# Kernel tuning notes

Measured on AMD Instinct MI355X. Metric: run time of the kernel, lower is better.

## Reference

```python
import jax, jax.numpy as jnp
import numpy as np

B, L, D, H = 2, 2048, 1024, 16
DH = D // H


def setup_inputs() -> dict:
    key = jax.random.key(0)
    ks = jax.random.split(key, 12)
    s = 0.02
    return {
        "q": jax.random.normal(ks[0], (B, L, D), jnp.float32),
        "k": jax.random.normal(ks[1], (B, L, D), jnp.float32),
        "v": jax.random.normal(ks[2], (B, L, D), jnp.float32),
        "pos_enc": jax.random.normal(ks[3], (L + 1, D), jnp.float32),
        "Wq": jax.random.normal(ks[4], (D, D), jnp.float32) * s,
        "bq": jnp.zeros((D,), jnp.float32),
        "Wk": jax.random.normal(ks[5], (D, D), jnp.float32) * s,
        "bk": jnp.zeros((D,), jnp.float32),
        "Wv": jax.random.normal(ks[6], (D, D), jnp.float32) * s,
        "bv": jnp.zeros((D,), jnp.float32),
        "Wo": jax.random.normal(ks[7], (D, D), jnp.float32) * s,
        "bo": jnp.zeros((D,), jnp.float32),
        "r_w_bias": jax.random.normal(ks[8], (H, 1, DH), jnp.float32) * s,
        "r_r_bias": jax.random.normal(ks[9], (H, 1, DH), jnp.float32) * s,
        "r_kernel": jax.random.normal(ks[10], (H, D, DH), jnp.float32) * s,
    }


def reference(q, k, v, pos_enc, Wq, bq, Wk, bk, Wv, bv, Wo, bo,
              r_w_bias, r_r_bias, r_kernel):
    b, lq, d = q.shape
    h, _, dh = r_w_bias.shape
    lk = k.shape[1]
    scale = dh ** -0.5

    # q/k/v projections, then split heads: [b, l, d] -> [b, h, l, dh]
    qh = (q @ Wq + bq).reshape(b, lq, h, dh).transpose(0, 2, 1, 3)
    kh = (k @ Wk + bk).reshape(b, lk, h, dh).transpose(0, 2, 1, 3)
    vh = (v @ Wv + bv).reshape(b, lk, h, dh).transpose(0, 2, 1, 3)

    # content scores with global content bias (Transformer-XL r_w_bias)
    scores = jnp.einsum('bhqd,bhkd->bhqk', qh + r_w_bias, kh) * scale

    # relative-position term: pos_enc [p, d] @ r_kernel [h, d, dh] -> [h, p, dh]
    pe = jnp.einsum('pd,hde->hpe', pos_enc, r_kernel)
    rel = jnp.einsum('bhqd,hpd->bhqp', qh + r_r_bias, pe) * scale  # [b,h,lq,p]
    p = rel.shape[-1]
    shift = 1 + (lq != lk)
    # rel-shift trick: reshape with swapped last two dims, drop first `shift`
    # rows, reshape back, keep first lk columns
    rel = rel.reshape(b, h, p, lq)[:, :, shift:, :]
    rel = rel.reshape(b, h, lq, p - shift)[..., :lk]
    scores = scores + rel

    # causal mask (key_cache is None path): subtract 1e7 on strict upper triangle
    causal_mask = jnp.triu(jnp.ones((lq, lk), dtype=bool), 1)
    scores = scores - causal_mask * 1e7

    out = jnp.einsum('bhqk,bhkd->bhqd', jax.nn.softmax(scores, axis=-1), vh)
    out = out.transpose(0, 2, 1, 3).reshape(b, lq, d)  # merge heads
    return out @ Wo + bo
```

## Files before the change

### kernel.cpp

```cpp
#include <hip/hip_runtime.h>
#include <hip/hip_bf16.h>

typedef __attribute__((ext_vector_type(8))) short bf16x8;
typedef __attribute__((ext_vector_type(4))) float f32x4;
typedef __attribute__((ext_vector_type(16))) float f32x16;
typedef unsigned short u16;
typedef unsigned int u32;

#define DEV static __device__ __forceinline__

DEV u16 f2us(float x) {
  __hip_bfloat16 h = __float2bfloat16(x);
  union { __hip_bfloat16 h; u16 u; } c; c.h = h; return c.u;
}
DEV float us2f(u16 u) {
  union { __hip_bfloat16 h; u16 u; } c; c.u = u;
  return __bfloat162float(c.h);
}
DEV f32x16 mfma32(bf16x8 a, bf16x8 b, f32x16 c) {
  return __builtin_amdgcn_mfma_f32_32x32x16_bf16(a, b, c, 0, 0, 0);
}
DEV u32 pkbf(float a, float b) {
  return (u32)f2us(a) | ((u32)f2us(b) << 16);
}
DEV void gl16(const u16* g, u16* l) {
  __builtin_amdgcn_global_load_lds(
      (const __attribute__((address_space(1))) unsigned int*)(g),
      (__attribute__((address_space(3))) unsigned int*)(l), 16, 0, 0);
}

constexpr int PE_ROWS = 2144;
constexpr int PE_M    = 2176;
constexpr float QSCALE = 0.125f;

constexpr size_t SZ_QKV  = (size_t)4096 * 1024 * 2;
constexpr size_t SZ_W    = (size_t)1024 * 1024 * 2;
constexpr size_t SZ_POSB = (size_t)PE_M * 1024 * 2;
constexpr size_t OFF_QB   = 0;
constexpr size_t OFF_KB   = OFF_QB  + SZ_QKV;
constexpr size_t OFF_VB   = OFF_KB  + SZ_QKV;
constexpr size_t OFF_WQT  = OFF_VB  + SZ_QKV;
constexpr size_t OFF_WKT  = OFF_WQT + SZ_W;
constexpr size_t OFF_WVT  = OFF_WKT + SZ_W;
constexpr size_t OFF_WOT  = OFF_WVT + SZ_W;
constexpr size_t OFF_RKT  = OFF_WOT + SZ_W;
constexpr size_t OFF_POSB = OFF_RKT + SZ_W;
constexpr size_t OFF_QW   = OFF_POSB + SZ_POSB;
constexpr size_t OFF_QR   = OFF_QW  + SZ_QKV;
constexpr size_t OFF_KH   = OFF_QR  + SZ_QKV;
constexpr size_t OFF_VT   = OFF_KH  + SZ_QKV;
constexpr size_t OFF_PEH  = OFF_VT  + SZ_QKV;
constexpr size_t OFF_ATTNB = OFF_QB;

__global__ __launch_bounds__(256)
void k_f2b_all(const float4* __restrict__ q, const float4* __restrict__ k,
               const float4* __restrict__ v, const float4* __restrict__ pos,
               u16* __restrict__ qb, u16* __restrict__ kb,
               u16* __restrict__ vb, u16* __restrict__ posb)
{
  const int bid = blockIdx.x;
  const float4* src; u16* dst; int i; int n4in, n4tot;
  if (bid < 4096)       { src = q;   dst = qb;   i = bid * 256 + threadIdx.x;           n4in = 1048576; n4tot = 1048576; }
  else if (bid < 8192)  { src = k;   dst = kb;   i = (bid - 4096) * 256 + threadIdx.x;  n4in = 1048576; n4tot = 1048576; }
  else if (bid < 12288) { src = v;   dst = vb;   i = (bid - 8192) * 256 + threadIdx.x;  n4in = 1048576; n4tot = 1048576; }
  else                  { src = pos; dst = posb; i = (bid - 12288) * 256 + threadIdx.x; n4in = 524544;  n4tot = 557056; }
  if (i >= n4tot) return;
  float4 val;
  if (i < n4in) val = src[i];
  else { val.x = val.y = val.z = val.w = 0.f; }
  ushort4 o;
  o.x = f2us(val.x); o.y = f2us(val.y); o.z = f2us(val.z); o.w = f2us(val.w);
  *reinterpret_cast<ushort4*>(dst + (size_t)i * 4) = o;
}

struct TcPtrs { const float *i0, *i1, *i2, *i3; u16 *o0, *o1, *o2, *o3; };

__global__ __launch_bounds__(256)
void k_tconv4(TcPtrs tp)
{
  const int z = blockIdx.z;
  const float* in = (z == 0) ? tp.i0 : (z == 1) ? tp.i1 : (z == 2) ? tp.i2 : tp.i3;
  u16* out = (z == 0) ? tp.o0 : (z == 1) ? tp.o1 : (z == 2) ? tp.o2 : tp.o3;
  __shared__ float t[32][33];
  const int kb0 = blockIdx.x * 32, nb0 = blockIdx.y * 32;
  const int tx = threadIdx.x & 31, ty = threadIdx.x >> 5;
#pragma unroll
  for (int r = 0; r < 32; r += 8)
    t[ty + r][tx] = in[(size_t)(kb0 + ty + r) * 1024 + nb0 + tx];
  __syncthreads();
#pragma unroll
  for (int r = 0; r < 32; r += 8)
    out[(size_t)(nb0 + ty + r) * 1024 + kb0 + tx] = f2us(t[tx][ty + r]);
}

__global__ __launch_bounds__(256)
void k_rkt(const float* __restrict__ rk, u16* __restrict__ out) {
  __shared__ float t[32][33];
  const int h = blockIdx.z;
  const int eb0 = blockIdx.x * 32, db0 = blockIdx.y * 32;
  const int tx = threadIdx.x & 31, ty = threadIdx.x >> 5;
#pragma unroll
  for (int r = 0; r < 32; r += 8)
    t[ty + r][tx] = rk[(size_t)h * 65536 + (size_t)(db0 + ty + r) * 64 + eb0 + tx];
  __syncthreads();
#pragma unroll
  for (int r = 0; r < 32; r += 8)
    out[(size_t)(h * 64 + eb0 + ty + r) * 1024 + db0 + tx] = f2us(t[tx][ty + r]);
}

struct ProjPtrs {
  const u16 *A0, *A1, *A2, *A3;
  const u16 *B0, *B1, *B2, *B3;
  const float *bias0, *bias1, *bias2;
  const float *rwb, *rrb;
  u16 *Qw, *Qr, *Kh, *Vt, *PEh;
};

__global__ __launch_bounds__(256)
void k_gemm_proj(ProjPtrs pp)
{
  const int z = blockIdx.z;
  if (z == 3 && blockIdx.y >= PE_M / 128) return;
  const u16* A  = (z == 0) ? pp.A0 : (z == 1) ? pp.A1 : (z == 2) ? pp.A2 : pp.A3;
  const u16* Bt = (z == 0) ? pp.B0 : (z == 1) ? pp.B1 : (z == 2) ? pp.B2 : pp.B3;

  __shared__ __attribute__((aligned(16))) u16 As[128 * 32];
  __shared__ __attribute__((aligned(16))) u16 Bs[128 * 32];
  const int tid  = threadIdx.x;
  const int lane = tid & 63;
  const int wave = tid >> 6;
  const int bm = blockIdx.y * 128;
  const int bn = blockIdx.x * 128;
  const int wr = (wave >> 1) * 64;
  const int wc = (wave & 1) * 64;
  const int fr = lane & 15;
  const int fk = (lane >> 4) * 8;

  f32x4 zero = {0.f, 0.f, 0.f, 0.f};
  f32x4 acc[4][4];
#pragma unroll
  for (int m = 0; m < 4; ++m)
#pragma unroll
    for (int n = 0; n < 4; ++n) acc[m][n] = zero;

  const int cA = wave * 2;
  const u16* gA = A  + (size_t)(bm + cA * 16 + (lane >> 2)) * 1024 + (lane & 3) * 8;
  const u16* gB = Bt + (size_t)(bn + cA * 16 + (lane >> 2)) * 1024 + (lane & 3) * 8;
  u16* lA = As + cA * 512;
  u16* lB = Bs + cA * 512;

  for (int k0 = 0; k0 < 1024; k0 += 32) {
    gl16(gA + k0, lA);
    gl16(gA + 16 * 1024 + k0, lA + 512);
    gl16(gB + k0, lB);
    gl16(gB + 16 * 1024 + k0, lB + 512);
    __syncthreads();
    bf16x8 af[4], bfv[4];
#pragma unroll
    for (int m = 0; m < 4; ++m) af[m]  = *(const bf16x8*)(&As[(wr + m * 16 + fr) * 32 + fk]);
#pragma unroll
    for (int n = 0; n < 4; ++n) bfv[n] = *(const bf16x8*)(&Bs[(wc + n * 16 + fr) * 32 + fk]);
#pragma unroll
    for (int m = 0; m < 4; ++m)
#pragma unroll
      for (int n = 0; n < 4; ++n)
        acc[m][n] = __builtin_amdgcn_mfma_f32_16x16x32_bf16(af[m], bfv[n], acc[m][n], 0, 0, 0);
    __syncthreads();
  }

#pragma unroll
  for (int m = 0; m < 4; ++m)
#pragma unroll
    for (int n = 0; n < 4; ++n)
#pragma unroll
      for (int r = 0; r < 4; ++r) {
        const int grow = bm + wr + m * 16 + (lane >> 4) * 4 + r;
        const int gcol = bn + wc + n * 16 + fr;
        float v = acc[m][n][r];
        const int b_ = grow >> 11, l_ = grow & 2047;
        const int h_ = gcol >> 6,  e_ = gcol & 63;
        if (z == 0) {
          v += pp.bias0[gcol];
          const size_t o = (((size_t)(b_ * 16 + h_) * 2048 + l_) << 6) + e_;
          pp.Qw[o] = f2us((v + pp.rwb[gcol]) * QSCALE);
          pp.Qr[o] = f2us((v + pp.rrb[gcol]) * QSCALE);
        } else if (z == 1) {
          v += pp.bias1[gcol];
          const size_t o = (((size_t)(b_ * 16 + h_) * 2048 + l_) << 6) + e_;
          pp.Kh[o] = f2us(v);
        } else if (z == 2) {
          v += pp.bias2[gcol];
          const size_t o = (((size_t)(b_ * 16 + h_) * 64 + e_) << 11) + l_;
          pp.Vt[o] = f2us(v);
        } else {
          if (grow < PE_ROWS) {
            const size_t o = ((size_t)h_ * PE_ROWS + grow) * 64 + e_;
            pp.PEh[o] = f2us(v);
          }
        }
      }
}

__global__ __launch_bounds__(256)
void k_gemm_o(const u16* __restrict__ A, const u16* __restrict__ Bt,
              const float* __restrict__ bias, float* __restrict__ outf)
{
  __shared__ __attribute__((aligned(16))) u16 As[128 * 32];
  __shared__ __attribute__((aligned(16))) u16 Bs[128 * 32];
  const int tid  = threadIdx.x;
  const int lane = tid & 63;
  const int wave = tid >> 6;
  const int bm = blockIdx.y * 128;
  const int bn = blockIdx.x * 128;
  const int wr = (wave >> 1) * 64;
  const int wc = (wave & 1) * 64;
  const int fr = lane & 15;
  const int fk = (lane >> 4) * 8;

  f32x4 zero = {0.f, 0.f, 0.f, 0.f};
  f32x4 acc[4][4];
#pragma unroll
  for (int m = 0; m < 4; ++m)
#pragma unroll
    for (int n = 0; n < 4; ++n) acc[m][n] = zero;

  const int cA = wave * 2;
  const u16* gA = A  + (size_t)(bm + cA * 16 + (lane >> 2)) * 1024 + (lane & 3) * 8;
  const u16* gB = Bt + (size_t)(bn + cA * 16 + (lane >> 2)) * 1024 + (lane & 3) * 8;
  u16* lA = As + cA * 512;
  u16* lB = Bs + cA * 512;

  for (int k0 = 0; k0 < 1024; k0 += 32) {
    gl16(gA + k0, lA);
    gl16(gA + 16 * 1024 + k0, lA + 512);
    gl16(gB + k0, lB);
    gl16(gB + 16 * 1024 + k0, lB + 512);
    __syncthreads();
    bf16x8 af[4], bfv[4];
#pragma unroll
    for (int m = 0; m < 4; ++m) af[m]  = *(const bf16x8*)(&As[(wr + m * 16 + fr) * 32 + fk]);
#pragma unroll
    for (int n = 0; n < 4; ++n) bfv[n] = *(const bf16x8*)(&Bs[(wc + n * 16 + fr) * 32 + fk]);
#pragma unroll
    for (int m = 0; m < 4; ++m)
#pragma unroll
      for (int n = 0; n < 4; ++n)
        acc[m][n] = __builtin_amdgcn_mfma_f32_16x16x32_bf16(af[m], bfv[n], acc[m][n], 0, 0, 0);
    __syncthreads();
  }

#pragma unroll
  for (int m = 0; m < 4; ++m)
#pragma unroll
    for (int n = 0; n < 4; ++n)
#pragma unroll
      for (int r = 0; r < 4; ++r) {
        const int grow = bm + wr + m * 16 + (lane >> 4) * 4 + r;
        const int gcol = bn + wc + n * 16 + fr;
        outf[(size_t)grow * 1024 + gcol] = acc[m][n][r] + bias[gcol];
      }
}


#define PV_HALF(WARR)                                                          \
  {                                                                            \
    _Pragma("unroll")                                                          \
    for (int kvs = 0; kvs < 2; ++kvs) {                                        \
      u32 snd0 = hi ? WARR[4 * kvs]     : WARR[4 * kvs + 2];                   \
      u32 snd1 = hi ? WARR[4 * kvs + 1] : WARR[4 * kvs + 3];                   \
      u32 r0 = (u32)__shfl_xor((int)snd0, 32);                                 \
      u32 r1 = (u32)__shfl_xor((int)snd1, 32);                                 \
      union { u32 u[4]; bf16x8 v; } pf;                                        \
      pf.u[0] = hi ? r0 : WARR[4 * kvs];                                       \
      pf.u[1] = hi ? r1 : WARR[4 * kvs + 1];                                   \
      pf.u[2] = hi ? WARR[4 * kvs + 2] : r0;                                   \
      pf.u[3] = hi ? WARR[4 * kvs + 3] : r1;                                   \
      bf16x8 v0_ = *(const bf16x8*)(V_h + (size_t)l31 * 2048 + c0h_            \
                                    + kvs * 16 + hi * 8);                      \
      bf16x8 v1_ = *(const bf16x8*)(V_h + (size_t)(32 + l31) * 2048 + c0h_     \
                                    + kvs * 16 + hi * 8);                      \
      Oc0 = mfma32(v0_, pf.v, Oc0);                                            \
      Oc1 = mfma32(v1_, pf.v, Oc1);                                            \
    }                                                                          \
  }

#define ATTN_HALF(q0v, c0_, KT)                                                \
  {                                                                            \
    const int c0h_ = (c0_) + (KT) * 32;                                        \
    f32x16 sv_ = {};                                                           \
    {                                                                          \
      bf16x8 kf_[4];                                                           \
      _Pragma("unroll")                                                        \
      for (int kk = 0; kk < 4; ++kk)                                           \
        kf_[kk] = *(const bf16x8*)(K_h + (size_t)(c0h_ + l31) * 64 + kk * 16   \
                                   + hi * 8);                                  \
      _Pragma("unroll")                                                        \
      for (int kk = 0; kk < 4; ++kk) sv_ = mfma32(kf_[kk], qwf[kk], sv_);      \
    }                                                                          \
    _Pragma("unroll")                                                          \
    for (int r = 0; r < 16; ++r) {                                             \
      const int pat = (r & 3) + 8 * (r >> 2) + 4 * hi;                         \
      float x = sv_[r] + us2f(Ew[l31][(KT) * 32 + pat + 31 - l31]);            \
      if (c0h_ + pat > (q0v) + l31) x = -1e30f;                                \
      sv_[r] = x;                                                              \
    }                                                                          \
    float mx_ = sv_[0];                                                        \
    _Pragma("unroll")                                                          \
    for (int r = 1; r < 16; ++r) mx_ = fmaxf(mx_, sv_[r]);                     \
    mx_ = fmaxf(mx_, __shfl_xor(mx_, 32));                                     \
    const float mn_ = fmaxf(mrun, mx_);                                        \
    const float al_ = __expf(mrun - mn_);                                      \
    mrun = mn_;                                                                \
    float rsum_ = 0.f;                                                         \
    u32 wa_[8];                                                                \
    _Pragma("unroll")                                                          \
    for (int g8 = 0; g8 < 8; ++g8) {                                           \
      float pa_ = __expf(sv_[2 * g8] - mn_);                                   \
      float pb_ = __expf(sv_[2 * g8 + 1] - mn_);                               \
      u16 ua_ = f2us(pa_), ub_ = f2us(pb_);                                    \
      rsum_ += us2f(ua_) + us2f(ub_);                                          \
      wa_[g8] = (u32)ua_ | ((u32)ub_ << 16);                                   \
    }                                                                          \
    ls = ls * al_ + rsum_ + __shfl_xor(rsum_, 32);                             \
    Oc0 *= al_;                                                                \
    Oc1 *= al_;                                                                \
    PV_HALF(wa_)                                                               \
  }

#define ATTN_STEP(q0v, stv)                                                    \
  {                                                                            \
    const int c0_ = (stv) * 64;                                                \
    const int Jb_ = 2048 + c0_ - (q0v) - 31;                                   \
    _Pragma("unroll")                                                          \
    for (int tau = 0; tau < 3; ++tau) {                                        \
      f32x16 e_ = {};                                                          \
      {                                                                        \
        bf16x8 pe_[4];                                                         \
        _Pragma("unroll")                                                      \
        for (int kk = 0; kk < 4; ++kk)                                         \
          pe_[kk] = *(const bf16x8*)(PE_h + (size_t)(Jb_ + tau * 32 + l31)     \
                                     * 64 + kk * 16 + hi * 8);                 \
        _Pragma("unroll")                                                      \
        for (int kk = 0; kk < 4; ++kk) e_ = mfma32(pe_[kk], qrf[kk], e_);      \
      }                                                                        \
      _Pragma("unroll")                                                        \
      for (int g4 = 0; g4 < 4; ++g4) {                                         \
        uint2 w2_;                                                             \
        w2_.x = pkbf(e_[4 * g4 + 0], e_[4 * g4 + 1]);                          \
        w2_.y = pkbf(e_[4 * g4 + 2], e_[4 * g4 + 3]);                          \
        *(uint2*)(&Ew[l31][tau * 32 + 8 * g4 + 4 * hi]) = w2_;                 \
      }                                                                        \
    }                                                                          \
    ATTN_HALF(q0v, c0_, 0)                                                     \
    ATTN_HALF(q0v, c0_, 1)                                                     \
  }

#define OBROUND(PRE, SCL)                                                      \
  {                                                                            \
    _Pragma("unroll")                                                          \
    for (int g4 = 0; g4 < 4; ++g4) {                                           \
      float* pb0 = &Obuf[l31][8 * g4 + 4 * hi];                                \
      float* pb1 = &Obuf[l31][32 + 8 * g4 + 4 * hi];                           \
      float2 a0 = *(float2*)pb0,       a1 = *(float2*)(pb0 + 2);               \
      float2 b0 = *(float2*)pb1,       b1 = *(float2*)(pb1 + 2);               \
      a0.x = a0.x * (PRE) + Oc0[4 * g4 + 0] * (SCL);                           \
      a0.y = a0.y * (PRE) + Oc0[4 * g4 + 1] * (SCL);                           \
      a1.x = a1.x * (PRE) + Oc0[4 * g4 + 2] * (SCL);                           \
      a1.y = a1.y * (PRE) + Oc0[4 * g4 + 3] * (SCL);                           \
      b0.x = b0.x * (PRE) + Oc1[4 * g4 + 0] * (SCL);                           \
      b0.y = b0.y * (PRE) + Oc1[4 * g4 + 1] * (SCL);                           \
      b1.x = b1.x * (PRE) + Oc1[4 * g4 + 2] * (SCL);                           \
      b1.y = b1.y * (PRE) + Oc1[4 * g4 + 3] * (SCL);                           \
      *(float2*)pb0 = a0; *(float2*)(pb0 + 2) = a1;                            \
      *(float2*)pb1 = b0; *(float2*)(pb1 + 2) = b1;                            \
    }                                                                          \
  }

__global__ __launch_bounds__(256, 4)
void k_attn(const u16* __restrict__ Qw, const u16* __restrict__ Qr,
            const u16* __restrict__ Kh, const u16* __restrict__ Vt,
            const u16* __restrict__ PEh, u16* __restrict__ attnb)
{
  const int bid = blockIdx.x;
  const int xcd = bid & 7, s = bid >> 3;
  const int p = s & 31, g = s >> 5;
  const int hb = xcd + 8 * g;
  const int h = hb & 15, b = hb >> 4;
  const int wave = threadIdx.x >> 6, lane = threadIdx.x & 63;
  const int l31 = lane & 31, hi = lane >> 5;

  const int qtL = 63 - p, qtS = p;
  const int q0L = qtL * 32, q0S = qtS * 32;
  const int nstL = qtL / 2 + 1;

  const u16* Qw_h = Qw + (size_t)hb * (2048 * 64);
  const u16* Qr_h = Qr + (size_t)hb * (2048 * 64);
  const u16* K_h  = Kh + (size_t)hb * (2048 * 64);
  const u16* V_h  = Vt + (size_t)hb * (64 * 2048);
  const u16* PE_h = PEh + (size_t)h * (PE_ROWS * 64);

  __shared__ __attribute__((aligned(16))) u16 Elds_all[4][32][100];
  __shared__ float Obuf[32][66];
  __shared__ float mlb[2][4][2][32];
  u16 (*Ew)[100] = Elds_all[wave];

  const int lo  = wave ? 9 + 8 * (wave - 1) : 0;
  const int hiE = lo + (wave ? 8 : 9);
  const int la0 = lo;
  const int la1 = hiE < nstL ? hiE : nstL;
  const int lb0 = lo > nstL ? lo : nstL;
  const int lb1 = hiE;
  const bool hasL = la1 > la0;
  const bool hasS = lb1 > lb0;
  const bool crossing = hasL && hasS;

  const f32x16 vzero = {};
  f32x16 Oc0 = {}, Oc1 = {};
  float mrun = -1e30f, ls = 0.f;
  bf16x8 qwf[4], qrf[4];

  if (hasL) {
#pragma unroll
    for (int kk = 0; kk < 4; ++kk) {
      qwf[kk] = *(const bf16x8*)(Qw_h + (size_t)(q0L + l31) * 64 + kk * 16 + hi * 8);
      qrf[kk] = *(const bf16x8*)(Qr_h + (size_t)(q0L + l31) * 64 + kk * 16 + hi * 8);
    }
    for (int st = la0; st < la1; ++st) ATTN_STEP(q0L, st)
  }
  if (crossing) {
    OBROUND(0.f, 1.f)
    if (hi == 0) { mlb[0][wave][0][l31] = mrun; mlb[0][wave][1][l31] = ls; }
    Oc0 = vzero; Oc1 = vzero; mrun = -1e30f; ls = 0.f;
  }
  if (hasS) {
#pragma unroll
    for (int kk = 0; kk < 4; ++kk) {
      qwf[kk] = *(const bf16x8*)(Qw_h + (size_t)(q0S + l31) * 64 + kk * 16 + hi * 8);
      qrf[kk] = *(const bf16x8*)(Qr_h + (size_t)(q0S + l31) * 64 + kk * 16 + hi * 8);
    }
    for (int st = lb0 - nstL; st < lb1 - nstL; ++st) ATTN_STEP(q0S, st)
  }

  if (hi == 0) {
    if (crossing) {
      mlb[1][wave][0][l31] = mrun; mlb[1][wave][1][l31] = ls;
    } else if (hasL) {
      mlb[0][wave][0][l31] = mrun;  mlb[0][wave][1][l31] = ls;
      mlb[1][wave][0][l31] = -1e30f; mlb[1][wave][1][l31] = 0.f;
    } else {
      mlb[1][wave][0][l31] = mrun;  mlb[1][wave][1][l31] = ls;
      mlb[0][wave][0][l31] = -1e30f; mlb[0][wave][1][l31] = 0.f;
    }
  }
  __syncthreads();

  const bool cwExists = (nstL != 17) && (nstL != 25);
  const int  cw = (nstL < 25) ? 2 : 3;

  const float mstL = fmaxf(fmaxf(mlb[0][0][0][l31], mlb[0][1][0][l31]),
                           fmaxf(mlb[0][2][0][l31], mlb[0][3][0][l31]));
  if (wave == 0) {
    const float preL = cwExists ? __expf(mlb[0][cw][0][l31] - mstL) : 0.f;
    const float scl = __expf(mrun - mstL);
    OBROUND(preL, scl)
  }
  __syncthreads();
  if (wave == 1) {
    const float scl = __expf(mrun - mstL);
    OBROUND(1.f, scl)
  }
  __syncthreads();
  if (wave == 2 && hasL && !crossing) {
    const float scl = __expf(mrun - mstL);
    OBROUND(1.f, scl)
  }
  __syncthreads();
  if (wave == 0) {
    float lst = 0.f;
#pragma unroll
    for (int w = 0; w < 4; ++w)
      lst += mlb[0][w][1][l31] * __expf(mlb[0][w][0][l31] - mstL);
    const float inv = 1.f / lst;
    const size_t orow = ((size_t)(b * 2048 + q0L + l31)) * 1024 + h * 64 + hi * 32;
#pragma unroll
    for (int j4 = 0; j4 < 32; j4 += 4) {
      float2 t0 = *(float2*)&Obuf[l31][hi * 32 + j4];
      float2 t1 = *(float2*)&Obuf[l31][hi * 32 + j4 + 2];
      ushort4 st;
      st.x = f2us(t0.x * inv); st.y = f2us(t0.y * inv);
      st.z = f2us(t1.x * inv); st.w = f2us(t1.y * inv);
      *(ushort4*)(attnb + orow + j4) = st;
    }
  }
  __syncthreads();

  const float mstS = fmaxf(mlb[1][2][0][l31], mlb[1][3][0][l31]);
  if (wave == 2 && hasS) {
    const float scl = __expf(mrun - mstS);
    OBROUND(0.f, scl)
  }
  __syncthreads();
  if (wave == 3) {
    const float scl = __expf(mrun - mstS);
    const float pre = (nstL < 25) ? 1.f : 0.f;
    OBROUND(pre, scl)
  }
  __syncthreads();
  if (wave == 1) {
    float lst = mlb[1][2][1][l31] * __expf(mlb[1][2][0][l31] - mstS)
              + mlb[1][3][1][l31] * __expf(mlb[1][3][0][l31] - mstS);
    const float inv = 1.f / lst;
    const size_t orow = ((size_t)(b * 2048 + q0S + l31)) * 1024 + h * 64 + hi * 32;
#pragma unroll
    for (int j4 = 0; j4 < 32; j4 += 4) {
      float2 t0 = *(float2*)&Obuf[l31][hi * 32 + j4];
      float2 t1 = *(float2*)&Obuf[l31][hi * 32 + j4 + 2];
      ushort4 st;
      st.x = f2us(t0.x * inv); st.y = f2us(t0.y * inv);
      st.z = f2us(t1.x * inv); st.w = f2us(t1.y * inv);
      *(ushort4*)(attnb + orow + j4) = st;
    }
  }
}

extern "C" void kernel_launch(void* const* d_in, const int* in_sizes, int n_in,
                              void* d_out, int out_size, void* d_ws, size_t ws_size,
                              hipStream_t stream)
{
  const float* q   = (const float*)d_in[0];
  const float* k   = (const float*)d_in[1];
  const float* v   = (const float*)d_in[2];
  const float* pos = (const float*)d_in[3];
  const float* Wq  = (const float*)d_in[4];
  const float* bq  = (const float*)d_in[5];
  const float* Wk  = (const float*)d_in[6];
  const float* bk  = (const float*)d_in[7];
  const float* Wv  = (const float*)d_in[8];
  const float* bv  = (const float*)d_in[9];
  const float* Wo  = (const float*)d_in[10];
  const float* bo  = (const float*)d_in[11];
  const float* rwb = (const float*)d_in[12];
  const float* rrb = (const float*)d_in[13];
  const float* rk  = (const float*)d_in[14];

  char* ws = (char*)d_ws;
  u16* qb    = (u16*)(ws + OFF_QB);
  u16* kb    = (u16*)(ws + OFF_KB);
  u16* vb    = (u16*)(ws + OFF_VB);
  u16* Wqt   = (u16*)(ws + OFF_WQT);
  u16* Wkt   = (u16*)(ws + OFF_WKT);
  u16* Wvt   = (u16*)(ws + OFF_WVT);
  u16* Wot   = (u16*)(ws + OFF_WOT);
  u16* Rkt   = (u16*)(ws + OFF_RKT);
  u16* posb  = (u16*)(ws + OFF_POSB);
  u16* Qw    = (u16*)(ws + OFF_QW);
  u16* Qr    = (u16*)(ws + OFF_QR);
  u16* Kh    = (u16*)(ws + OFF_KH);
  u16* Vt    = (u16*)(ws + OFF_VT);
  u16* PEh   = (u16*)(ws + OFF_PEH);
  u16* attnb = (u16*)(ws + OFF_ATTNB);
  float* outf = (float*)d_out;

  k_f2b_all<<<dim3(14464), 256, 0, stream>>>((const float4*)q, (const float4*)k,
                                             (const float4*)v, (const float4*)pos,
                                             qb, kb, vb, posb);
  TcPtrs tp;
  tp.i0 = Wq; tp.i1 = Wk; tp.i2 = Wv; tp.i3 = Wo;
  tp.o0 = Wqt; tp.o1 = Wkt; tp.o2 = Wvt; tp.o3 = Wot;
  k_tconv4<<<dim3(32, 32, 4), 256, 0, stream>>>(tp);
  k_rkt<<<dim3(2, 32, 16), 256, 0, stream>>>(rk, Rkt);

  ProjPtrs pp;
  pp.A0 = qb;  pp.A1 = kb;  pp.A2 = vb;  pp.A3 = posb;
  pp.B0 = Wqt; pp.B1 = Wkt; pp.B2 = Wvt; pp.B3 = Rkt;
  pp.bias0 = bq; pp.bias1 = bk; pp.bias2 = bv;
  pp.rwb = rwb; pp.rrb = rrb;
  pp.Qw = Qw; pp.Qr = Qr; pp.Kh = Kh; pp.Vt = Vt; pp.PEh = PEh;
  k_gemm_proj<<<dim3(8, 32, 4), 256, 0, stream>>>(pp);

  k_attn<<<dim3(1024), 256, 0, stream>>>(Qw, Qr, Kh, Vt, PEh, attnb);

  k_gemm_o<<<dim3(8, 32), 256, 0, stream>>>(attnb, Wot, bo, outf);
}
```

Baseline: 247.4 us.

## Merge prep kernels, reuse rel-pos tile across steps, use exp2 and mask skip

Folds the three preprocessing launches (bf16 conversion, weight transposes, r_kernel transpose) into a single kernel to save launch overhead. In attention, the third positional-encoding tile of each step is kept in registers and reused as the first tile of the next step, so each step computes two PE MFMA tiles instead of three. Causal masking is skipped for tiles entirely below the diagonal, V fragments are loaded early next to the K loads, and the softmax uses v_exp_f32 (exp2) with log2(e) folded into the Q scale. The stray label in the Rkt loop looks odd but is harmless; the cross-step register carry adds register pressure.

```diff
diff --git a/kernel.cpp b/kernel.cpp
--- a/kernel.cpp
+++ b/kernel.cpp
@@ -23,6 +23,11 @@
 DEV u32 pkbf(float a, float b) {
   return (u32)f2us(a) | ((u32)f2us(b) << 16);
 }
+DEV float fexp2(float x) {
+  float r;
+  asm("v_exp_f32 %0, %1" : "=v"(r) : "v"(x));
+  return r;
+}
 DEV void gl16(const u16* g, u16* l) {
   __builtin_amdgcn_global_load_lds(
       (const __attribute__((address_space(1))) unsigned int*)(g),
@@ -31,7 +36,7 @@
 
 constexpr int PE_ROWS = 2144;
 constexpr int PE_M    = 2176;
-constexpr float QSCALE = 0.125f;
+constexpr float QSC2 = 0.125f * 1.4426950408889634f;
 
 constexpr size_t SZ_QKV  = (size_t)4096 * 1024 * 2;
 constexpr size_t SZ_W    = (size_t)1024 * 1024 * 2;
@@ -52,60 +57,62 @@
 constexpr size_t OFF_PEH  = OFF_VT  + SZ_QKV;
 constexpr size_t OFF_ATTNB = OFF_QB;
 
+struct PrepPtrs {
+  const float4 *q, *k, *v, *pos;
+  u16 *qb, *kb, *vb, *posb;
+  const float *Wq, *Wk, *Wv, *Wo, *rk;
+  u16 *Wqt, *Wkt, *Wvt, *Wot, *Rkt;
+};
+
 __global__ __launch_bounds__(256)
-void k_f2b_all(const float4* __restrict__ q, const float4* __restrict__ k,
-               const float4* __restrict__ v, const float4* __restrict__ pos,
-               u16* __restrict__ qb, u16* __restrict__ kb,
-               u16* __restrict__ vb, u16* __restrict__ posb)
+void k_prep(PrepPtrs P)
 {
+  __shared__ float t[32][33];
   const int bid = blockIdx.x;
-  const float4* src; u16* dst; int i; int n4in, n4tot;
-  if (bid < 4096)       { src = q;   dst = qb;   i = bid * 256 + threadIdx.x;           n4in = 1048576; n4tot = 1048576; }
-  else if (bid < 8192)  { src = k;   dst = kb;   i = (bid - 4096) * 256 + threadIdx.x;  n4in = 1048576; n4tot = 1048576; }
-  else if (bid < 12288) { src = v;   dst = vb;   i = (bid - 8192) * 256 + threadIdx.x;  n4in = 1048576; n4tot = 1048576; }
-  else                  { src = pos; dst = posb; i = (bid - 12288) * 256 + threadIdx.x; n4in = 524544;  n4tot = 557056; }
-  if (i >= n4tot) return;
-  float4 val;
-  if (i < n4in) val = src[i];
-  else { val.x = val.y = val.z = val.w = 0.f; }
-  ushort4 o;
-  o.x = f2us(val.x); o.y = f2us(val.y); o.z = f2us(val.z); o.w = f2us(val.w);
-  *reinterpret_cast<ushort4*>(dst + (size_t)i * 4) = o;
-}
-
-struct TcPtrs { const float *i0, *i1, *i2, *i3; u16 *o0, *o1, *o2, *o3; };
-
-__global__ __launch_bounds__(256)
-void k_tconv4(TcPtrs tp)
-{
-  const int z = blockIdx.z;
-  const float* in = (z == 0) ? tp.i0 : (z == 1) ? tp.i1 : (z == 2) ? tp.i2 : tp.i3;
-  u16* out = (z == 0) ? tp.o0 : (z == 1) ? tp.o1 : (z == 2) ? tp.o2 : tp.o3;
-  __shared__ float t[32][33];
-  const int kb0 = blockIdx.x * 32, nb0 = blockIdx.y * 32;
+  if (bid < 14464) {
+    const float4* src; u16* dst; int i, n4in, n4tot;
+    if (bid < 4096)       { src = P.q;   dst = P.qb;   i = bid * 256 + threadIdx.x;           n4in = 1048576; n4tot = 1048576; }
+    else if (bid < 8192)  { src = P.k;   dst = P.kb;   i = (bid - 4096) * 256 + threadIdx.x;  n4in = 1048576; n4tot = 1048576; }
+    else if (bid < 12288) { src = P.v;   dst = P.vb;   i = (bid - 8192) * 256 + threadIdx.x;  n4in = 1048576; n4tot = 1048576; }
+    else                  { src = P.pos; dst = P.posb; i = (bid - 12288) * 256 + threadIdx.x; n4in = 524544;  n4tot = 557056; }
+    if (i >= n4tot) return;
+    float4 val;
+    if (i < n4in) val = src[i];
+    else { val.x = val.y = val.z = val.w = 0.f; }
+    ushort4 o;
+    o.x = f2us(val.x); o.y = f2us(val.y); o.z = f2us(val.z); o.w = f2us(val.w);
+    *reinterpret_cast<ushort4*>(dst + (size_t)i * 4) = o;
+    return;
+  }
   const int tx = threadIdx.x & 31, ty = threadIdx.x >> 5;
-#pragma unroll
-  for (int r = 0; r < 32; r += 8)
-    t[ty + r][tx] = in[(size_t)(kb0 + ty + r) * 1024 + nb0 + tx];
-  __syncthreads();
-#pragma unroll
-  for (int r = 0; r < 32; r += 8)
-    out[(size_t)(nb0 + ty + r) * 1024 + kb0 + tx] = f2us(t[tx][ty + r]);
-}
-
-__global__ __launch_bounds__(256)
-void k_rkt(const float* __restrict__ rk, u16* __restrict__ out) {
-  __shared__ float t[32][33];
-  const int h = blockIdx.z;
-  const int eb0 = blockIdx.x * 32, db0 = blockIdx.y * 32;
-  const int tx = threadIdx.x & 31, ty = threadIdx.x >> 5;
-#pragma unroll
-  for (int r = 0; r < 32; r += 8)
-    t[ty + r][tx] = rk[(size_t)h * 65536 + (size_t)(db0 + ty + r) * 64 + eb0 + tx];
-  __syncthreads();
-#pragma unroll
-  for (int r = 0; r < 32; r += 8)
-    out[(size_t)(h * 64 + eb0 + ty + r) * 1024 + db0 + tx] = f2us(t[tx][ty + r]);
+  if (bid < 18560) {
+    const int tt = bid - 14464;
+    const int z = tt >> 10, rr = tt & 1023;
+    const float* in = (z == 0) ? P.Wq : (z == 1) ? P.Wk : (z == 2) ? P.Wv : P.Wo;
+    u16* out = (z == 0) ? P.Wqt : (z == 1) ? P.Wkt : (z == 2) ? P.Wvt : P.Wot;
+    const int kb0 = (rr & 31) * 32, nb0 = (rr >> 5) * 32;
+#pragma unroll
+    for (int r = 0; r < 32; r += 8)
+      t[ty + r][tx] = in[(size_t)(kb0 + ty + r) * 1024 + nb0 + tx];
+    __syncthreads();
+#pragma unroll
+    for (int r = 0; r < 32; r += 8)
+      out[(size_t)(nb0 + ty + r) * 1024 + kb0 + tx] = f2us(t[tx][ty + r]);
+    return;
+  }
+  {
+    const int tt = bid - 18560;
+    const int e = tt & 1, d = (tt >> 1) & 31, h = tt >> 6;
+    const int eb0 = e * 32, db0 = d * 32;
+#pragma unroll
+    for (int r = 0; r < 32; r += 8)
+      t[ty + r][tx] = P.rk[(size_t)h * 65536 + (size_t)(db0 + ty + r) * 64 + eb0 + tx];
+    __syncthreads();
+#pragma unroll
+    for (int r = 0; r < 32; r += 8)
+      out_rkt_store:
+      P.Rkt[(size_t)(h * 64 + eb0 + ty + r) * 1024 + db0 + tx] = f2us(t[tx][ty + r]);
+  }
 }
 
 struct ProjPtrs {
@@ -182,8 +189,8 @@
         if (z == 0) {
           v += pp.bias0[gcol];
           const size_t o = (((size_t)(b_ * 16 + h_) * 2048 + l_) << 6) + e_;
-          pp.Qw[o] = f2us((v + pp.rwb[gcol]) * QSCALE);
-          pp.Qr[o] = f2us((v + pp.rrb[gcol]) * QSCALE);
+          pp.Qw[o] = f2us((v + pp.rwb[gcol]) * QSC2);
+          pp.Qr[o] = f2us((v + pp.rrb[gcol]) * QSC2);
         } else if (z == 1) {
           v += pp.bias1[gcol];
           const size_t o = (((size_t)(b_ * 16 + h_) * 2048 + l_) << 6) + e_;
@@ -262,61 +269,55 @@
 }
 
 
-#define PV_HALF(WARR)                                                          \
-  {                                                                            \
-    _Pragma("unroll")                                                          \
-    for (int kvs = 0; kvs < 2; ++kvs) {                                        \
-      u32 snd0 = hi ? WARR[4 * kvs]     : WARR[4 * kvs + 2];                   \
-      u32 snd1 = hi ? WARR[4 * kvs + 1] : WARR[4 * kvs + 3];                   \
-      u32 r0 = (u32)__shfl_xor((int)snd0, 32);                                 \
-      u32 r1 = (u32)__shfl_xor((int)snd1, 32);                                 \
-      union { u32 u[4]; bf16x8 v; } pf;                                        \
-      pf.u[0] = hi ? r0 : WARR[4 * kvs];                                       \
-      pf.u[1] = hi ? r1 : WARR[4 * kvs + 1];                                   \
-      pf.u[2] = hi ? WARR[4 * kvs + 2] : r0;                                   \
-      pf.u[3] = hi ? WARR[4 * kvs + 3] : r1;                                   \
-      bf16x8 v0_ = *(const bf16x8*)(V_h + (size_t)l31 * 2048 + c0h_            \
-                                    + kvs * 16 + hi * 8);                      \
-      bf16x8 v1_ = *(const bf16x8*)(V_h + (size_t)(32 + l31) * 2048 + c0h_     \
-                                    + kvs * 16 + hi * 8);                      \
-      Oc0 = mfma32(v0_, pf.v, Oc0);                                            \
-      Oc1 = mfma32(v1_, pf.v, Oc1);                                            \
-    }                                                                          \
-  }
-
 #define ATTN_HALF(q0v, c0_, KT)                                                \
   {                                                                            \
     const int c0h_ = (c0_) + (KT) * 32;                                        \
     f32x16 sv_ = {};                                                           \
+    bf16x8 vpa_[4];                                                            \
     {                                                                          \
       bf16x8 kf_[4];                                                           \
       _Pragma("unroll")                                                        \
       for (int kk = 0; kk < 4; ++kk)                                           \
         kf_[kk] = *(const bf16x8*)(K_h + (size_t)(c0h_ + l31) * 64 + kk * 16   \
                                    + hi * 8);                                  \
+      vpa_[0] = *(const bf16x8*)(V_h + (size_t)l31 * 2048 + c0h_ + hi * 8);    \
+      vpa_[1] = *(const bf16x8*)(V_h + (size_t)(32 + l31) * 2048 + c0h_        \
+                                 + hi * 8);                                    \
+      vpa_[2] = *(const bf16x8*)(V_h + (size_t)l31 * 2048 + c0h_ + 16          \
+                                 + hi * 8);                                    \
+      vpa_[3] = *(const bf16x8*)(V_h + (size_t)(32 + l31) * 2048 + c0h_ + 16   \
+                                 + hi * 8);                                    \
       _Pragma("unroll")                                                        \
       for (int kk = 0; kk < 4; ++kk) sv_ = mfma32(kf_[kk], qwf[kk], sv_);      \
     }                                                                          \
-    _Pragma("unroll")                                                          \
-    for (int r = 0; r < 16; ++r) {                                             \
-      const int pat = (r & 3) + 8 * (r >> 2) + 4 * hi;                         \
-      float x = sv_[r] + us2f(Ew[l31][(KT) * 32 + pat + 31 - l31]);            \
-      if (c0h_ + pat > (q0v) + l31) x = -1e30f;                                \
-      sv_[r] = x;                                                              \
+    if (c0h_ + 31 > (q0v)) {                                                   \
+      _Pragma("unroll")                                                        \
+      for (int r = 0; r < 16; ++r) {                                           \
+        const int pat = (r & 3) + 8 * (r >> 2) + 4 * hi;                       \
+        float x = sv_[r] + us2f(Ew[l31][(KT) * 32 + pat + 31 - l31]);          \
+        if (c0h_ + pat > (q0v) + l31) x = -1e30f;                              \
+        sv_[r] = x;                                                            \
+      }                                                                        \
+    } else {                                                                   \
+      _Pragma("unroll")                                                        \
+      for (int r = 0; r < 16; ++r) {                                           \
+        const int pat = (r & 3) + 8 * (r >> 2) + 4 * hi;                       \
+        sv_[r] += us2f(Ew[l31][(KT) * 32 + pat + 31 - l31]);                   \
+      }                                                                        \
     }                                                                          \
     float mx_ = sv_[0];                                                        \
     _Pragma("unroll")                                                          \
     for (int r = 1; r < 16; ++r) mx_ = fmaxf(mx_, sv_[r]);                     \
     mx_ = fmaxf(mx_, __shfl_xor(mx_, 32));                                     \
     const float mn_ = fmaxf(mrun, mx_);                                        \
-    const float al_ = __expf(mrun - mn_);                                      \
+    const float al_ = fexp2(mrun - mn_);                                       \
     mrun = mn_;                                                                \
     float rsum_ = 0.f;                                                         \
     u32 wa_[8];                                                                \
     _Pragma("unroll")                                                          \
     for (int g8 = 0; g8 < 8; ++g8) {                                           \
-      float pa_ = __expf(sv_[2 * g8] - mn_);                                   \
-      float pb_ = __expf(sv_[2 * g8 + 1] - mn_);                               \
+      float pa_ = fexp2(sv_[2 * g8] - mn_);                                    \
+      float pb_ = fexp2(sv_[2 * g8 + 1] - mn_);                                \
       u16 ua_ = f2us(pa_), ub_ = f2us(pb_);                                    \
       rsum_ += us2f(ua_) + us2f(ub_);                                          \
       wa_[g8] = (u32)ua_ | ((u32)ub_ << 16);                                   \
@@ -324,7 +325,40 @@
     ls = ls * al_ + rsum_ + __shfl_xor(rsum_, 32);                             \
     Oc0 *= al_;                                                                \
     Oc1 *= al_;                                                                \
-    PV_HALF(wa_)                                                               \
+    _Pragma("unroll")                                                          \
+    for (int kvs = 0; kvs < 2; ++kvs) {                                        \
+      u32 snd0 = hi ? wa_[4 * kvs]     : wa_[4 * kvs + 2];                     \
+      u32 snd1 = hi ? wa_[4 * kvs + 1] : wa_[4 * kvs + 3];                     \
+      u32 r0 = (u32)__shfl_xor((int)snd0, 32);                                 \
+      u32 r1 = (u32)__shfl_xor((int)snd1, 32);                                 \
+      union { u32 u[4]; bf16x8 v; } pf;                                        \
+      pf.u[0] = hi ? r0 : wa_[4 * kvs];                                        \
+      pf.u[1] = hi ? r1 : wa_[4 * kvs + 1];                                    \
+      pf.u[2] = hi ? wa_[4 * kvs + 2] : r0;                                    \
+      pf.u[3] = hi ? wa_[4 * kvs + 3] : r1;                                    \
+      Oc0 = mfma32(vpa_[2 * kvs], pf.v, Oc0);                                  \
+      Oc1 = mfma32(vpa_[2 * kvs + 1], pf.v, Oc1);                              \
+    }                                                                          \
+  }
+
+#define SEG_PROLOGUE(q0v, s0v)                                                 \
+  {                                                                            \
+    const int Jb_ = 2048 + (s0v) * 64 - (q0v) - 31;                            \
+    f32x16 e_ = {};                                                            \
+    {                                                                          \
+      bf16x8 pe_[4];                                                           \
+      _Pragma("unroll")                                                        \
+      for (int kk = 0; kk < 4; ++kk)                                           \
+        pe_[kk] = *(const bf16x8*)(PE_h + (size_t)(Jb_ + l31) * 64 + kk * 16   \
+                                   + hi * 8);                                  \
+      _Pragma("unroll")                                                        \
+      for (int kk = 0; kk < 4; ++kk) e_ = mfma32(pe_[kk], qrf[kk], e_);        \
+    }                                                                          \
+    _Pragma("unroll")                                                          \
+    for (int g4 = 0; g4 < 4; ++g4) {                                           \
+      cr[2 * g4]     = pkbf(e_[4 * g4 + 0], e_[4 * g4 + 1]);                   \
+      cr[2 * g4 + 1] = pkbf(e_[4 * g4 + 2], e_[4 * g4 + 3]);                   \
+    }                                                                          \
   }
 
 #define ATTN_STEP(q0v, stv)                                                    \
@@ -332,14 +366,18 @@
     const int c0_ = (stv) * 64;                                                \
     const int Jb_ = 2048 + c0_ - (q0v) - 31;                                   \
     _Pragma("unroll")                                                          \
-    for (int tau = 0; tau < 3; ++tau) {                                        \
+    for (int g4 = 0; g4 < 4; ++g4) {                                           \
+      uint2 w2_; w2_.x = cr[2 * g4]; w2_.y = cr[2 * g4 + 1];                   \
+      *(uint2*)(&Ew[l31][8 * g4 + 4 * hi]) = w2_;                              \
+    }                                                                          \
+    {                                                                          \
       f32x16 e_ = {};                                                          \
       {                                                                        \
         bf16x8 pe_[4];                                                         \
         _Pragma("unroll")                                                      \
         for (int kk = 0; kk < 4; ++kk)                                         \
-          pe_[kk] = *(const bf16x8*)(PE_h + (size_t)(Jb_ + tau * 32 + l31)     \
-                                     * 64 + kk * 16 + hi * 8);                 \
+          pe_[kk] = *(const bf16x8*)(PE_h + (size_t)(Jb_ + 32 + l31) * 64      \
+                                     + kk * 16 + hi * 8);                      \
         _Pragma("unroll")                                                      \
         for (int kk = 0; kk < 4; ++kk) e_ = mfma32(pe_[kk], qrf[kk], e_);      \
       }                                                                        \
@@ -348,7 +386,26 @@
         uint2 w2_;                                                             \
         w2_.x = pkbf(e_[4 * g4 + 0], e_[4 * g4 + 1]);                          \
         w2_.y = pkbf(e_[4 * g4 + 2], e_[4 * g4 + 3]);                          \
-        *(uint2*)(&Ew[l31][tau * 32 + 8 * g4 + 4 * hi]) = w2_;                 \
+        *(uint2*)(&Ew[l31][32 + 8 * g4 + 4 * hi]) = w2_;                       \
+      }                                                                        \
+    }                                                                          \
+    {                                                                          \
+      f32x16 e_ = {};                                                          \
+      {                                                                        \
+        bf16x8 pe_[4];                                                         \
+        _Pragma("unroll")                                                      \
+        for (int kk = 0; kk < 4; ++kk)                                         \
+          pe_[kk] = *(const bf16x8*)(PE_h + (size_t)(Jb_ + 64 + l31) * 64      \
+                                     + kk * 16 + hi * 8);                      \
+        _Pragma("unroll")                                                      \
+        for (int kk = 0; kk < 4; ++kk) e_ = mfma32(pe_[kk], qrf[kk], e_);      \
+      }                                                                        \
+      _Pragma("unroll")                                                        \
+      for (int g4 = 0; g4 < 4; ++g4) {                                         \
+        cr[2 * g4]     = pkbf(e_[4 * g4 + 0], e_[4 * g4 + 1]);                 \
+        cr[2 * g4 + 1] = pkbf(e_[4 * g4 + 2], e_[4 * g4 + 3]);                 \
+        uint2 w2_; w2_.x = cr[2 * g4]; w2_.y = cr[2 * g4 + 1];                 \
+        *(uint2*)(&Ew[l31][64 + 8 * g4 + 4 * hi]) = w2_;                       \
       }                                                                        \
     }                                                                          \
     ATTN_HALF(q0v, c0_, 0)                                                     \
@@ -418,6 +475,7 @@
   f32x16 Oc0 = {}, Oc1 = {};
   float mrun = -1e30f, ls = 0.f;
   bf16x8 qwf[4], qrf[4];
+  u32 cr[8];
 
   if (hasL) {
 #pragma unroll
@@ -425,6 +483,7 @@
       qwf[kk] = *(const bf16x8*)(Qw_h + (size_t)(q0L + l31) * 64 + kk * 16 + hi * 8);
       qrf[kk] = *(const bf16x8*)(Qr_h + (size_t)(q0L + l31) * 64 + kk * 16 + hi * 8);
     }
+    SEG_PROLOGUE(q0L, la0)
     for (int st = la0; st < la1; ++st) ATTN_STEP(q0L, st)
   }
   if (crossing) {
@@ -438,6 +497,7 @@
       qwf[kk] = *(const bf16x8*)(Qw_h + (size_t)(q0S + l31) * 64 + kk * 16 + hi * 8);
       qrf[kk] = *(const bf16x8*)(Qr_h + (size_t)(q0S + l31) * 64 + kk * 16 + hi * 8);
     }
+    SEG_PROLOGUE(q0S, lb0 - nstL)
     for (int st = lb0 - nstL; st < lb1 - nstL; ++st) ATTN_STEP(q0S, st)
   }
 
@@ -460,18 +520,18 @@
   const float mstL = fmaxf(fmaxf(mlb[0][0][0][l31], mlb[0][1][0][l31]),
                            fmaxf(mlb[0][2][0][l31], mlb[0][3][0][l31]));
   if (wave == 0) {
-    const float preL = cwExists ? __expf(mlb[0][cw][0][l31] - mstL) : 0.f;
-    const float scl = __expf(mrun - mstL);
+    const float preL = cwExists ? fexp2(mlb[0][cw][0][l31] - mstL) : 0.f;
+    const float scl = fexp2(mrun - mstL);
     OBROUND(preL, scl)
   }
   __syncthreads();
   if (wave == 1) {
-    const float scl = __expf(mrun - mstL);
+    const float scl = fexp2(mrun - mstL);
     OBROUND(1.f, scl)
   }
   __syncthreads();
   if (wave == 2 && hasL && !crossing) {
-    const float scl = __expf(mrun - mstL);
+    const float scl = fexp2(mrun - mstL);
     OBROUND(1.f, scl)
   }
   __syncthreads();
@@ -479,7 +539,7 @@
     float lst = 0.f;
 #pragma unroll
     for (int w = 0; w < 4; ++w)
-      lst += mlb[0][w][1][l31] * __expf(mlb[0][w][0][l31] - mstL);
+      lst += mlb[0][w][1][l31] * fexp2(mlb[0][w][0][l31] - mstL);
     const float inv = 1.f / lst;
     const size_t orow = ((size_t)(b * 2048 + q0L + l31)) * 1024 + h * 64 + hi * 32;
 #pragma unroll
@@ -496,19 +556,19 @@
 
   const float mstS = fmaxf(mlb[1][2][0][l31], mlb[1][3][0][l31]);
   if (wave == 2 && hasS) {
-    const float scl = __expf(mrun - mstS);
+    const float scl = fexp2(mrun - mstS);
     OBROUND(0.f, scl)
   }
   __syncthreads();
   if (wave == 3) {
-    const float scl = __expf(mrun - mstS);
+    const float scl = fexp2(mrun - mstS);
     const float pre = (nstL < 25) ? 1.f : 0.f;
     OBROUND(pre, scl)
   }
   __syncthreads();
   if (wave == 1) {
-    float lst = mlb[1][2][1][l31] * __expf(mlb[1][2][0][l31] - mstS)
-              + mlb[1][3][1][l31] * __expf(mlb[1][3][0][l31] - mstS);
+    float lst = mlb[1][2][1][l31] * fexp2(mlb[1][2][0][l31] - mstS)
+              + mlb[1][3][1][l31] * fexp2(mlb[1][3][0][l31] - mstS);
     const float inv = 1.f / lst;
     const size_t orow = ((size_t)(b * 2048 + q0S + l31)) * 1024 + h * 64 + hi * 32;
 #pragma unroll
@@ -561,14 +621,13 @@
   u16* attnb = (u16*)(ws + OFF_ATTNB);
   float* outf = (float*)d_out;
 
-  k_f2b_all<<<dim3(14464), 256, 0, stream>>>((const float4*)q, (const float4*)k,
-                                             (const float4*)v, (const float4*)pos,
-                                             qb, kb, vb, posb);
-  TcPtrs tp;
-  tp.i0 = Wq; tp.i1 = Wk; tp.i2 = Wv; tp.i3 = Wo;
-  tp.o0 = Wqt; tp.o1 = Wkt; tp.o2 = Wvt; tp.o3 = Wot;
-  k_tconv4<<<dim3(32, 32, 4), 256, 0, stream>>>(tp);
-  k_rkt<<<dim3(2, 32, 16), 256, 0, stream>>>(rk, Rkt);
+  PrepPtrs P;
+  P.q = (const float4*)q; P.k = (const float4*)k; P.v = (const float4*)v;
+  P.pos = (const float4*)pos;
+  P.qb = qb; P.kb = kb; P.vb = vb; P.posb = posb;
+  P.Wq = Wq; P.Wk = Wk; P.Wv = Wv; P.Wo = Wo; P.rk = rk;
+  P.Wqt = Wqt; P.Wkt = Wkt; P.Wvt = Wvt; P.Wot = Wot; P.Rkt = Rkt;
+  k_prep<<<dim3(19584), 256, 0, stream>>>(P);
 
   ProjPtrs pp;
   pp.A0 = qb;  pp.A1 = kb;  pp.A2 = vb;  pp.A3 = posb;
```

Measured after the change: 545.8 us. 2.21x slower.
